# Kernel tuning notes

Hardware: AMD Instinct MI355X
Metric: run time of the kernel (lower is better)

Reference implementation:

```python
import jax, jax.numpy as jnp
import numpy as np

N = 50000          # nodes
E = 800000         # edges (avg degree 16)
IN_DIM = 64        # input feature dim
HEADS = 8          # heads in hidden layers
T = 3              # num edge types
NUM_CLASSES = 16   # output layer: 1 head, hidden = num_classes
SLOPE = 0.2        # LeakyReLU negative slope


def typed_linear(x, etype, W):
    # x: [E, din], W: [T, din, dout] -> per-edge-type linear (grouped GEMM)
    out = jnp.zeros((x.shape[0], W.shape[2]), dtype=x.dtype)
    for t in range(W.shape[0]):  # small fixed loop over edge types
        out = out + jnp.where((etype == t)[:, None], x @ W[t], jnp.zeros((), x.dtype))
    return out


def edge_softmax(scores, dst, n):
    # segmented softmax over incoming edges of each dst node; scores: [E, H]
    m = jax.ops.segment_max(scores, dst, num_segments=n)
    e = jnp.exp(scores - m[dst])
    s = jax.ops.segment_sum(e, dst, num_segments=n)
    return e / s[dst]


def hetsann_conv(x, src, dst, etype, W, a_l, a_r, heads, res, act, n):
    ne = src.shape[0]
    m = x[src]                                   # copy_u: gather src features to edges
    feat = typed_linear(m, etype, W)             # [E, heads*d]
    d = feat.shape[1] // heads
    h_l = typed_linear(feat, etype, a_l).reshape(ne, heads, d).sum(-1)  # [E, H]
    h_r = typed_linear(feat, etype, a_r).reshape(ne, heads, d).sum(-1)  # [E, H]
    att = jax.nn.leaky_relu(h_l + h_r, SLOPE)    # [E, H]
    alpha = edge_softmax(att, dst, n)            # [E, H]
    # attention-weighted messages, scatter-summed to dst (HetSANN eq. 5)
    msg = (feat.reshape(ne, heads, d) * alpha[:, :, None]).reshape(ne, heads * d)
    out = jax.ops.segment_sum(msg, dst, num_segments=n)  # [N, heads*d]
    if res is not None:
        w, b = res
        out = out + x @ w + b
    if act:
        out = jax.nn.elu(out)
    return out


def setup_inputs() -> dict:
    key = jax.random.key(0)
    ks = jax.random.split(key, 14)
    s = 1.0 / np.sqrt(IN_DIM)
    s2 = 1.0 / np.sqrt(NUM_CLASSES)
    return {
        "x": jax.random.normal(ks[0], (N, IN_DIM), dtype=jnp.float32),
        "src": jax.random.randint(ks[1], (E,), 0, N),
        "dst": jax.random.randint(ks[2], (E,), 0, N),
        "ntype": jax.random.randint(ks[3], (N,), 0, T),
        "etype": jax.random.randint(ks[4], (E,), 0, T),
        # layer 0: TypedLinear(64 -> 64), heads=8
        "W1": jax.random.normal(ks[5], (T, IN_DIM, IN_DIM), dtype=jnp.float32) * s,
        "al1": jax.random.normal(ks[6], (T, IN_DIM, IN_DIM), dtype=jnp.float32) * s,
        "ar1": jax.random.normal(ks[7], (T, IN_DIM, IN_DIM), dtype=jnp.float32) * s,
        # layer 1 (output): TypedLinear(64 -> 16), heads=1, residual Linear(64 -> 16)
        "W2": jax.random.normal(ks[8], (T, IN_DIM, NUM_CLASSES), dtype=jnp.float32) * s,
        "al2": jax.random.normal(ks[9], (T, NUM_CLASSES, NUM_CLASSES), dtype=jnp.float32) * s2,
        "ar2": jax.random.normal(ks[10], (T, NUM_CLASSES, NUM_CLASSES), dtype=jnp.float32) * s2,
        "res_w": jax.random.normal(ks[11], (IN_DIM, NUM_CLASSES), dtype=jnp.float32) * s,
        "res_b": jax.random.normal(ks[12], (NUM_CLASSES,), dtype=jnp.float32) * 0.01,
    }


def reference(x, src, dst, ntype, etype, W1, al1, ar1, W2, al2, ar2, res_w, res_b):
    # layer 0: 8 heads, no residual, ELU activation (dropout=0 -> identity)
    h = hetsann_conv(x, src, dst, etype, W1, al1, ar1, HEADS, None, True, N)
    # output layer: 1 head, hidden=num_classes, residual, no activation
    h = hetsann_conv(h, src, dst, etype, W2, al2, ar2, 1, (res_w, res_b), False, N)
    # dgl.mean_nodes over the single graph
    return h.mean(axis=0)  # [NUM_CLASSES]
```

## Files before the change

### kernel.cpp

```cpp
#include <hip/hip_runtime.h>
#include <hip/hip_bf16.h>

typedef unsigned int u32;
typedef unsigned short u16;
typedef unsigned char u8;

#define NN 50000
#define EE 800000
#define TT 3
#define NBUCK 196
#define BSTRIDE 8192
#define P1_CHUNK 4096

#define OFF_C1     0
#define OFF_C2     1536
#define OFF_BCNT   1728
#define OFF_OPART  1984
#define OFF_BBASE  3008
#define OFF_ROWPTR 52756
#define OFF_CW1    102760
#define OFF_CW2    117096
#define OFF_PSRC   153016
#define OFF_PK1    953024
#define OFF_TMP    953024
#define OFF_PK2    953024
#define OFF_H      5753024

__device__ __forceinline__ float bf2f(u32 u) {
    union { u32 i; float f; } v; v.i = u << 16; return v.f;
}
__device__ __forceinline__ u32 f2bf(float f) {
    union { float f; u32 i; } v; v.f = f;
    return (v.i + 0x7fffu + ((v.i >> 16) & 1u)) >> 16;
}

__global__ void precompute(const float* __restrict__ W1, const float* __restrict__ al1,
                           const float* __restrict__ ar1, const float* __restrict__ W2,
                           const float* __restrict__ al2, const float* __restrict__ ar2,
                           float* __restrict__ ws) {
    __shared__ float a1c[64][8];
    __shared__ float a2c[16];
    int t = blockIdx.x;
    int tid = threadIdx.x;
    {
        int k2 = tid >> 3, hh = tid & 7;
        float s = 0.f;
#pragma unroll
        for (int j = 0; j < 8; ++j) {
            int idx = t * 4096 + k2 * 64 + hh * 8 + j;
            s += al1[idx] + ar1[idx];
        }
        a1c[k2][hh] = s;
    }
    if (tid < 16) {
        float s = 0.f;
#pragma unroll
        for (int j = 0; j < 16; ++j) {
            int idx = t * 256 + tid * 16 + j;
            s += al2[idx] + ar2[idx];
        }
        a2c[tid] = s;
    }
    __syncthreads();
    {
        int k = tid >> 3, hh = tid & 7;
        float s = 0.f;
#pragma unroll
        for (int k2 = 0; k2 < 64; ++k2)
            s += W1[t * 4096 + k * 64 + k2] * a1c[k2][hh];
        ws[OFF_C1 + t * 512 + k * 8 + hh] = s;
    }
    if (tid < 64) {
        float s = 0.f;
#pragma unroll
        for (int k2 = 0; k2 < 16; ++k2)
            s += W2[t * 1024 + tid * 16 + k2] * a2c[k2];
        ws[OFF_C2 + t * 64 + tid] = s;
    }
}

__global__ __launch_bounds__(256) void fill_cw(const float* __restrict__ W1, const float* __restrict__ W2,
                        const float* __restrict__ res_w, float* __restrict__ ws) {
    int idx = blockIdx.x * 256 + threadIdx.x;
    if (idx < 14336) {
        int k = idx / 224, c = idx - k * 224;
        float v;
        if (c < 192) v = W1[(c >> 6) * 4096 + k * 64 + (c & 63)];
        else if (c < 216) v = ws[OFF_C1 + ((c - 192) >> 3) * 512 + k * 8 + ((c - 192) & 7)];
        else v = 0.f;
        ws[OFF_CW1 + idx] = v;
    }
    if (idx < 4352) {
        int k = idx / 68, c = idx - k * 68;
        float v;
        if (c < 48) v = W2[(c >> 4) * 1024 + k * 16 + (c & 15)];
        else if (c < 51) v = ws[OFF_C2 + (c - 48) * 64 + k];
        else if (c < 67) v = res_w[k * 16 + (c - 51)];
        else v = 0.f;
        ws[OFF_CW2 + idx] = v;
    }
}

__global__ __launch_bounds__(256) void sort_p1(const int* __restrict__ src, const int* __restrict__ dst,
                        const int* __restrict__ etype, int* wsi) {
    __shared__ u32 Est[P1_CHUNK];
    __shared__ u8 Bst[P1_CHUNK];
    __shared__ int hist[NBUCK], base[NBUCK];
    int tid = threadIdx.x;
    int e0 = blockIdx.x * P1_CHUNK;
    int cnt = EE - e0; if (cnt > P1_CHUNK) cnt = P1_CHUNK;
    for (int i = tid; i < NBUCK; i += 256) hist[i] = 0;
    __syncthreads();
    for (int i = tid; i < cnt; i += 256) {
        int e = e0 + i;
        int s = src[e], d = dst[e], t = etype[e];
        int b = d >> 8;
        Est[i] = (u32)s | ((u32)t << 16) | ((u32)(d & 255) << 18);
        Bst[i] = (u8)b;
        atomicAdd(&hist[b], 1);
    }
    __syncthreads();
    for (int i = tid; i < NBUCK; i += 256) {
        int h = hist[i];
        base[i] = h ? atomicAdd(wsi + OFF_BCNT + i, h) : 0;
        hist[i] = 0;
    }
    __syncthreads();
    for (int i = tid; i < cnt; i += 256) {
        int b = Bst[i];
        int idx = base[b] + atomicAdd(&hist[b], 1);
        wsi[OFF_TMP + b * BSTRIDE + idx] = (int)Est[i];
    }
}

__global__ __launch_bounds__(256) void sort_p2a(int* wsi) {
    __shared__ int sd[256];
    int t = threadIdx.x;
    int v = (t < NBUCK) ? wsi[OFF_BCNT + t] : 0;
    sd[t] = v;
    __syncthreads();
    for (int o = 1; o < 256; o <<= 1) {
        int u = (t >= o) ? sd[t - o] : 0;
        __syncthreads();
        sd[t] += u;
        __syncthreads();
    }
    if (t < NBUCK) wsi[OFF_BBASE + t] = sd[t] - v;
    if (t == 0) wsi[OFF_ROWPTR + NN] = EE;
}

__global__ __launch_bounds__(256) void sort_p2(int* wsi) {
    __shared__ int cnt[256], sd[256], lrpx[256];
    int b = blockIdx.x;
    int tid = threadIdx.x;
    int nb = wsi[OFF_BCNT + b];
    int gbase = wsi[OFF_BBASE + b];
    cnt[tid] = 0;
    __syncthreads();
    const int* tmp = wsi + OFF_TMP + b * BSTRIDE;
    for (int i = tid; i < nb; i += 256) {
        int e = tmp[i];
        atomicAdd(&cnt[(e >> 18) & 255], 1);
    }
    __syncthreads();
    int v = cnt[tid];
    sd[tid] = v;
    __syncthreads();
    for (int o = 1; o < 256; o <<= 1) {
        int u = (tid >= o) ? sd[tid - o] : 0;
        __syncthreads();
        sd[tid] += u;
        __syncthreads();
    }
    int ex = sd[tid] - v;
    lrpx[tid] = ex;
    int d = b * 256 + tid;
    if (d < NN) wsi[OFF_ROWPTR + d] = gbase + ex;
    cnt[tid] = 0;
    __syncthreads();
    for (int i = tid; i < nb; i += 256) {
        int e = tmp[i];
        int dres = (e >> 18) & 255;
        int slot = gbase + lrpx[dres] + atomicAdd(&cnt[dres], 1);
        wsi[OFF_PSRC + slot] = (e & 0xFFFF) | (((e >> 16) & 3) << 20);
    }
}

__global__ __launch_bounds__(512) void gemm_f(const float* __restrict__ x, const float* __restrict__ cw,
                       float* __restrict__ ws) {
    __shared__ alignas(16) float Xs[64 * 65];
    int tid = threadIdx.x;
    int wave = __builtin_amdgcn_readfirstlane(tid >> 6);
    int lane = tid & 63;
    int n0 = blockIdx.x * 64;
    {
        const float4* xg = (const float4*)(x + (size_t)n0 * 64);
        for (int q = tid; q < 1024; q += 512) {
            int row = q >> 4;
            float4 v = (n0 + row < NN) ? xg[q] : make_float4(0.f, 0.f, 0.f, 0.f);
            *(float4*)(Xs + row * 65 + (q & 15) * 4) = v;
        }
    }
    __syncthreads();
    int cbase = wave * 28;
    float acc[28];
#pragma unroll
    for (int i = 0; i < 28; ++i) acc[i] = 0.f;
    const float* xrow = Xs + lane * 65;
    float wA[28], wB[28];
#pragma unroll
    for (int j = 0; j < 28; ++j) wA[j] = cw[cbase + j];
    for (int k = 0; k < 64; k += 2) {
#pragma unroll
        for (int j = 0; j < 28; ++j) wB[j] = cw[(k + 1) * 224 + cbase + j];
        float xv = xrow[k];
#pragma unroll
        for (int j = 0; j < 28; ++j) acc[j] = fmaf(xv, wA[j], acc[j]);
        if (k + 2 < 64) {
#pragma unroll
            for (int j = 0; j < 28; ++j) wA[j] = cw[(k + 2) * 224 + cbase + j];
        }
        float xv2 = xrow[k + 1];
#pragma unroll
        for (int j = 0; j < 28; ++j) acc[j] = fmaf(xv2, wB[j], acc[j]);
    }
    int n = n0 + lane;
    if (n < NN) {
        u32* row = (u32*)ws + OFF_PK1 + (size_t)n * 96;
#pragma unroll
        for (int g = 0; g < 7; ++g) {
            int col = cbase + 4 * g;
            float v0 = acc[4*g], v1 = acc[4*g+1], v2 = acc[4*g+2], v3 = acc[4*g+3];
            if (col < 192) {
                int t = col >> 6, ci = col & 63;
                int dw = __builtin_amdgcn_cvt_pk_fp8_f32(v0, v1, 0, false);
                dw = __builtin_amdgcn_cvt_pk_fp8_f32(v2, v3, dw, true);
                row[t * 32 + (ci >> 2)] = (u32)dw;
            } else if (col < 216) {
                int jj = col - 192;
                int t = jj >> 3, rem = jj & 7;
                v0 = v0 > 0.f ? v0 : 0.2f * v0;
                v1 = v1 > 0.f ? v1 : 0.2f * v1;
                v2 = v2 > 0.f ? v2 : 0.2f * v2;
                v3 = v3 > 0.f ? v3 : 0.2f * v3;
                row[t * 32 + 16 + (rem >> 1)]     = f2bf(__expf(v0)) | (f2bf(__expf(v1)) << 16);
                row[t * 32 + 16 + (rem >> 1) + 1] = f2bf(__expf(v2)) | (f2bf(__expf(v3)) << 16);
            }
        }
    }
}

__global__ __launch_bounds__(256) void agg1(const int* __restrict__ wsi, float* __restrict__ ws) {
    int tid = threadIdx.x;
    int wave = tid >> 6, lane = tid & 63;
    int q = lane >> 3;
    int cg = lane & 7;
    int d = blockIdx.x * 4 + wave;
    int epw = cg >> 1;
    int sh_ep = (cg & 1) * 16;
    int start = wsi[OFF_ROWPTR + d], end = wsi[OFF_ROWPTR + d + 1];
    const u32* pk = (const u32*)ws + OFF_PK1;
    const int* psrc = wsi + OFF_PSRC;
    float acc[8];
#pragma unroll
    for (int i = 0; i < 8; ++i) acc[i] = 0.f;
    float den = 0.f;
    int s = start + q;
    u32 f0_c = 0, f1_c = 0, ep_c = 0;
    int p1 = 0;
    bool valid = s < end;
    if (valid) {
        int p = psrc[s];
        int sn = p & 0xFFFFF, t = p >> 20;
        size_t base = (size_t)(sn * 3 + t) * 32;
        uint2 f = *(const uint2*)(pk + base + 2 * cg);
        f0_c = f.x; f1_c = f.y;
        ep_c = pk[base + 16 + epw];
    }
    if (s + 8 < end) p1 = psrc[s + 8];
    while (valid) {
        u32 f0 = f0_c, f1 = f1_c, ep = ep_c;
        bool v1 = s + 8 < end;
        if (v1) {
            int sn = p1 & 0xFFFFF, t = p1 >> 20;
            size_t base = (size_t)(sn * 3 + t) * 32;
            uint2 f = *(const uint2*)(pk + base + 2 * cg);
            f0_c = f.x; f1_c = f.y;
            ep_c = pk[base + 16 + epw];
        }
        if (s + 16 < end) p1 = psrc[s + 16];
        float w = bf2f((ep >> sh_ep) & 0xffffu);
        den += w;
        acc[0] += w * __builtin_amdgcn_cvt_f32_fp8((int)f0, 0);
        acc[1] += w * __builtin_amdgcn_cvt_f32_fp8((int)(f0 >> 8), 0);
        acc[2] += w * __builtin_amdgcn_cvt_f32_fp8((int)(f0 >> 16), 0);
        acc[3] += w * __builtin_amdgcn_cvt_f32_fp8((int)(f0 >> 24), 0);
        acc[4] += w * __builtin_amdgcn_cvt_f32_fp8((int)f1, 0);
        acc[5] += w * __builtin_amdgcn_cvt_f32_fp8((int)(f1 >> 8), 0);
        acc[6] += w * __builtin_amdgcn_cvt_f32_fp8((int)(f1 >> 16), 0);
        acc[7] += w * __builtin_amdgcn_cvt_f32_fp8((int)(f1 >> 24), 0);
        s += 8;
        valid = v1;
    }
#pragma unroll
    for (int i = 0; i < 8; ++i) {
        acc[i] += __shfl_xor(acc[i], 8);
        acc[i] += __shfl_xor(acc[i], 16);
        acc[i] += __shfl_xor(acc[i], 32);
    }
    den += __shfl_xor(den, 8);
    den += __shfl_xor(den, 16);
    den += __shfl_xor(den, 32);
    if (q == 0) {
        float dn = (end > start) ? den : 1.f;
        float o[8];
#pragma unroll
        for (int i = 0; i < 8; ++i) {
            float v = acc[i] / dn;
            o[i] = v > 0.f ? v : __expf(v) - 1.f;
        }
        float* dst = ws + OFF_H + (size_t)d * 64 + cg * 8;
        *(float4*)dst       = make_float4(o[0], o[1], o[2], o[3]);
        *(float4*)(dst + 4) = make_float4(o[4], o[5], o[6], o[7]);
    }
}

__global__ __launch_bounds__(256) void gemm_f2(const float* __restrict__ cw, float* __restrict__ ws) {
    __shared__ alignas(16) float Hs[64 * 65];
    __shared__ float Rs[64][17];
    int tid = threadIdx.x;
    int wave = __builtin_amdgcn_readfirstlane(tid >> 6);
    int lane = tid & 63;
    int n0 = blockIdx.x * 64;
    {
        const float4* hg = (const float4*)(ws + OFF_H + (size_t)n0 * 64);
        for (int q = tid; q < 1024; q += 256) {
            int row = q >> 4;
            float4 v = (n0 + row < NN) ? hg[q] : make_float4(0.f, 0.f, 0.f, 0.f);
            *(float4*)(Hs + row * 65 + (q & 15) * 4) = v;
        }
    }
    __syncthreads();
    int cbase = wave * 17;
    float acc[17];
#pragma unroll
    for (int i = 0; i < 17; ++i) acc[i] = 0.f;
    const float* hrow = Hs + lane * 65;
    float wA[17], wB[17];
#pragma unroll
    for (int j = 0; j < 17; ++j) wA[j] = cw[cbase + j];
    for (int k = 0; k < 64; k += 2) {
#pragma unroll
        for (int j = 0; j < 17; ++j) wB[j] = cw[(k + 1) * 68 + cbase + j];
        float hv = hrow[k];
#pragma unroll
        for (int j = 0; j < 17; ++j) acc[j] = fmaf(hv, wA[j], acc[j]);
        if (k + 2 < 64) {
#pragma unroll
            for (int j = 0; j < 17; ++j) wA[j] = cw[(k + 2) * 68 + cbase + j];
        }
        float hv2 = hrow[k + 1];
#pragma unroll
        for (int j = 0; j < 17; ++j) acc[j] = fmaf(hv2, wB[j], acc[j]);
    }
    int n = n0 + lane;
    u16* pk2u = (u16*)((u32*)ws + OFF_PK2);
#pragma unroll
    for (int i = 0; i < 17; ++i) {
        int col = cbase + i;
        if (col < 48) {
            if (n < NN) {
                int t = col >> 4, c2 = col & 15;
                pk2u[((size_t)n * 3 + t) * 32 + c2] = (u16)f2bf(acc[i]);
            }
        } else if (col < 51) {
            if (n < NN) {
                float v = acc[i]; v = v > 0.f ? v : 0.2f * v;
                ws[OFF_PK2 + ((size_t)n * 3 + (col - 48)) * 16 + 8] = __expf(v);
            }
        } else if (col < 67) {
            Rs[lane][col - 51] = acc[i];
        }
    }
    __syncthreads();
    if (tid < 16) {
        float s = 0.f;
#pragma unroll 8
        for (int r = 0; r < 64; ++r) s += Rs[r][tid];
        atomicAdd(ws + OFF_OPART + (blockIdx.x & 63) * 16 + tid, s);
    }
}

__global__ __launch_bounds__(256) void agg2(const int* __restrict__ wsi, float* __restrict__ ws) {
    __shared__ float outs[4][16];
    int tid = threadIdx.x;
    int wave = tid >> 6, lane = tid & 63;
    int q = lane >> 4, c = lane & 15;
    int d = blockIdx.x * 4 + wave;
    int start = wsi[OFF_ROWPTR + d], end = wsi[OFF_ROWPTR + d + 1];
    const u16* pk2u = (const u16*)((const u32*)ws + OFF_PK2);
    const float* pk2f = ws + OFF_PK2;
    const int* psrc = wsi + OFF_PSRC;
    float acc = 0.f, den = 0.f;
    int s = start + q;
    float w_c = 0.f, m_c = 0.f;
    bool valid = s < end;
    if (valid) {
        int p = psrc[s];
        int sn = p & 0xFFFFF, t = p >> 20;
        size_t r = (size_t)(sn * 3 + t);
        w_c = pk2f[r * 16 + 8];
        m_c = bf2f(pk2u[r * 32 + c]);
    }
    while (valid) {
        float w = w_c, m = m_c;
        int s2 = s + 4;
        bool v2 = s2 < end;
        if (v2) {
            int p = psrc[s2];
            int sn = p & 0xFFFFF, t = p >> 20;
            size_t r = (size_t)(sn * 3 + t);
            w_c = pk2f[r * 16 + 8];
            m_c = bf2f(pk2u[r * 32 + c]);
        }
        den += w;
        acc += w * m;
        s = s2; valid = v2;
    }
    acc += __shfl_xor(acc, 16);
    acc += __shfl_xor(acc, 32);
    den += __shfl_xor(den, 16);
    den += __shfl_xor(den, 32);
    float val = (end > start) ? acc / den : 0.f;
    if (q == 0) outs[wave][c] = val;
    __syncthreads();
    if (tid < 16) {
        float sum = outs[0][tid] + outs[1][tid] + outs[2][tid] + outs[3][tid];
        atomicAdd(ws + OFF_OPART + (blockIdx.x & 63) * 16 + tid, sum);
    }
}

__global__ void final_k(const float* __restrict__ res_b, float* __restrict__ ws, float* __restrict__ out) {
    int c = threadIdx.x;
    if (c < 16) {
        float s = 0.f;
        for (int r = 0; r < 64; ++r) s += ws[OFF_OPART + r * 16 + c];
        out[c] = s * (1.0f / (float)NN) + res_b[c];
    }
}

extern "C" void kernel_launch(void* const* d_in, const int* in_sizes, int n_in,
                              void* d_out, int out_size, void* d_ws, size_t ws_size,
                              hipStream_t stream) {
    const float* x     = (const float*)d_in[0];
    const int*   src   = (const int*)d_in[1];
    const int*   dst   = (const int*)d_in[2];
    const int*   etype = (const int*)d_in[4];
    const float* W1    = (const float*)d_in[5];
    const float* al1   = (const float*)d_in[6];
    const float* ar1   = (const float*)d_in[7];
    const float* W2    = (const float*)d_in[8];
    const float* al2   = (const float*)d_in[9];
    const float* ar2   = (const float*)d_in[10];
    const float* res_w = (const float*)d_in[11];
    const float* res_b = (const float*)d_in[12];
    float* ws = (float*)d_ws;
    int* wsi = (int*)d_ws;
    float* out = (float*)d_out;

    hipMemsetAsync((char*)d_ws + (size_t)OFF_BCNT * 4, 0, (size_t)1280 * 4, stream);
    hipLaunchKernelGGL(precompute, dim3(TT), dim3(512), 0, stream, W1, al1, ar1, W2, al2, ar2, ws);
    hipLaunchKernelGGL(fill_cw, dim3(56), dim3(256), 0, stream, W1, W2, res_w, ws);
    hipLaunchKernelGGL(sort_p1, dim3((EE + P1_CHUNK - 1) / P1_CHUNK), dim3(256), 0, stream, src, dst, etype, wsi);
    hipLaunchKernelGGL(sort_p2a, dim3(1), dim3(256), 0, stream, wsi);
    hipLaunchKernelGGL(sort_p2, dim3(NBUCK), dim3(256), 0, stream, wsi);
    hipLaunchKernelGGL(gemm_f, dim3((NN + 63) / 64), dim3(512), 0, stream, x, ws + OFF_CW1, ws);
    hipLaunchKernelGGL(agg1, dim3(NN / 4), dim3(256), 0, stream, wsi, ws);
    hipLaunchKernelGGL(gemm_f2, dim3((NN + 63) / 64), dim3(256), 0, stream, ws + OFF_CW2, ws);
    hipLaunchKernelGGL(agg2, dim3(NN / 4), dim3(256), 0, stream, wsi, ws);
    hipLaunchKernelGGL(final_k, dim3(1), dim3(64), 0, stream, res_b, ws, out);
}
```

Before: 253.9 us.

## Restructure first GEMM so each lane holds one weight column in registers

The node-feature GEMM no longer stages a 64-node tile of x in shared memory with 28 accumulators per lane. Each lane now keeps one full 64-entry weight column in registers and loops over 32 nodes, reading x rows with wave-uniform (broadcast) loads. Each lane writes single fp8 bytes or bf16 halves instead of packed dwords. This removes the LDS staging and barrier, but it leaves 8 of 64 lanes idle, does more global x loads, and makes the stores narrow and scattered.

```diff
diff --git a/kernel.cpp b/kernel.cpp
--- a/kernel.cpp
+++ b/kernel.cpp
@@ -11,6 +11,7 @@
 #define NBUCK 196
 #define BSTRIDE 8192
 #define P1_CHUNK 4096
+#define NPB 32
 
 #define OFF_C1     0
 #define OFF_C2     1536
@@ -186,65 +187,40 @@
     }
 }
 
-__global__ __launch_bounds__(512) void gemm_f(const float* __restrict__ x, const float* __restrict__ cw,
+__global__ __launch_bounds__(256) void gemm_f(const float* __restrict__ x, const float* __restrict__ cw,
                        float* __restrict__ ws) {
-    __shared__ alignas(16) float Xs[64 * 65];
     int tid = threadIdx.x;
     int wave = __builtin_amdgcn_readfirstlane(tid >> 6);
     int lane = tid & 63;
-    int n0 = blockIdx.x * 64;
-    {
-        const float4* xg = (const float4*)(x + (size_t)n0 * 64);
-        for (int q = tid; q < 1024; q += 512) {
-            int row = q >> 4;
-            float4 v = (n0 + row < NN) ? xg[q] : make_float4(0.f, 0.f, 0.f, 0.f);
-            *(float4*)(Xs + row * 65 + (q & 15) * 4) = v;
-        }
-    }
-    __syncthreads();
-    int cbase = wave * 28;
-    float acc[28];
-#pragma unroll
-    for (int i = 0; i < 28; ++i) acc[i] = 0.f;
-    const float* xrow = Xs + lane * 65;
-    float wA[28], wB[28];
-#pragma unroll
-    for (int j = 0; j < 28; ++j) wA[j] = cw[cbase + j];
-    for (int k = 0; k < 64; k += 2) {
-#pragma unroll
-        for (int j = 0; j < 28; ++j) wB[j] = cw[(k + 1) * 224 + cbase + j];
-        float xv = xrow[k];
-#pragma unroll
-        for (int j = 0; j < 28; ++j) acc[j] = fmaf(xv, wA[j], acc[j]);
-        if (k + 2 < 64) {
-#pragma unroll
-            for (int j = 0; j < 28; ++j) wA[j] = cw[(k + 2) * 224 + cbase + j];
-        }
-        float xv2 = xrow[k + 1];
-#pragma unroll
-        for (int j = 0; j < 28; ++j) acc[j] = fmaf(xv2, wB[j], acc[j]);
-    }
-    int n = n0 + lane;
-    if (n < NN) {
-        u32* row = (u32*)ws + OFF_PK1 + (size_t)n * 96;
-#pragma unroll
-        for (int g = 0; g < 7; ++g) {
-            int col = cbase + 4 * g;
-            float v0 = acc[4*g], v1 = acc[4*g+1], v2 = acc[4*g+2], v3 = acc[4*g+3];
-            if (col < 192) {
-                int t = col >> 6, ci = col & 63;
-                int dw = __builtin_amdgcn_cvt_pk_fp8_f32(v0, v1, 0, false);
-                dw = __builtin_amdgcn_cvt_pk_fp8_f32(v2, v3, dw, true);
-                row[t * 32 + (ci >> 2)] = (u32)dw;
-            } else if (col < 216) {
-                int jj = col - 192;
-                int t = jj >> 3, rem = jj & 7;
-                v0 = v0 > 0.f ? v0 : 0.2f * v0;
-                v1 = v1 > 0.f ? v1 : 0.2f * v1;
-                v2 = v2 > 0.f ? v2 : 0.2f * v2;
-                v3 = v3 > 0.f ? v3 : 0.2f * v3;
-                row[t * 32 + 16 + (rem >> 1)]     = f2bf(__expf(v0)) | (f2bf(__expf(v1)) << 16);
-                row[t * 32 + 16 + (rem >> 1) + 1] = f2bf(__expf(v2)) | (f2bf(__expf(v3)) << 16);
+    int cbase = wave * 56;
+    int mycol = cbase + lane;
+    bool colok = lane < 56;
+    float w[64];
+#pragma unroll
+    for (int k = 0; k < 64; ++k)
+        w[k] = colok ? cw[k * 224 + mycol] : 0.f;
+    int tt, ci, epbyte = 0;
+    bool isF = mycol < 192;
+    if (isF) { tt = mycol >> 6; ci = mycol & 63; }
+    else { int jj = mycol - 192; tt = jj >> 3; epbyte = tt * 128 + 64 + (jj & 7) * 2; }
+    bool doStore = colok && mycol < 216;
+    int n0 = blockIdx.x * NPB;
+    for (int ni = 0; ni < NPB; ++ni) {
+        int n = n0 + ni;
+        if (n >= NN) break;
+        const float* xrow = x + (size_t)n * 64;
+        float acc = 0.f;
+#pragma unroll
+        for (int k = 0; k < 64; ++k)
+            acc = fmaf(xrow[k], w[k], acc);
+        if (doStore) {
+            u8* rowb = (u8*)ws + ((size_t)OFF_PK1 + (size_t)n * 96) * 4;
+            if (isF) {
+                int b = __builtin_amdgcn_cvt_pk_fp8_f32(acc, acc, 0, false);
+                rowb[tt * 128 + ci] = (u8)(b & 0xff);
+            } else {
+                float v = acc > 0.f ? acc : 0.2f * acc;
+                *(u16*)(rowb + epbyte) = (u16)f2bf(__expf(v));
             }
         }
     }
@@ -474,7 +450,7 @@
     hipLaunchKernelGGL(sort_p1, dim3((EE + P1_CHUNK - 1) / P1_CHUNK), dim3(256), 0, stream, src, dst, etype, wsi);
     hipLaunchKernelGGL(sort_p2a, dim3(1), dim3(256), 0, stream, wsi);
     hipLaunchKernelGGL(sort_p2, dim3(NBUCK), dim3(256), 0, stream, wsi);
-    hipLaunchKernelGGL(gemm_f, dim3((NN + 63) / 64), dim3(512), 0, stream, x, ws + OFF_CW1, ws);
+    hipLaunchKernelGGL(gemm_f, dim3((NN + NPB - 1) / NPB), dim3(256), 0, stream, x, ws + OFF_CW1, ws);
     hipLaunchKernelGGL(agg1, dim3(NN / 4), dim3(256), 0, stream, wsi, ws);
     hipLaunchKernelGGL(gemm_f2, dim3((NN + 63) / 64), dim3(256), 0, stream, ws + OFF_CW2, ws);
     hipLaunchKernelGGL(agg2, dim3(NN / 4), dim3(256), 0, stream, wsi, ws);
```

New measurement: 255.7 us. No clear change (+0.7%).
